# Optimization experiments

Measured on AMD Instinct MI355X. Metric: run time of the kernel, lower is better.

The kernel has to match this reference:

```python
import jax, jax.numpy as jnp
import numpy as np

B, C, S, H, W = 2, 128, 64, 128, 512
MID = 32
EPS = 1e-5


def layer_norm(x, g, b):
    m = jnp.mean(x, axis=-1, keepdims=True)
    v = jnp.var(x, axis=-1, keepdims=True)
    return (x - m) / jnp.sqrt(v + EPS) * g + b


def generate_y_for_attn(s, y, u):
    # y: [B, Cy, H, W], u: [B, s, s] int indices into W (clamped)
    b, cy, h, w = y.shape
    u = jnp.clip(u, 0, w - 1)
    yr = y.reshape(b, cy * h, w)
    idx = u.reshape(b, s * s)
    g = jax.vmap(lambda m, i: m[:, i])(yr, idx)          # [B, Cy*H, s^2]
    return g.reshape(b, cy, h, s * s).transpose(0, 3, 2, 1)  # [B, s^2, H, Cy]


def setup_inputs():
    key = jax.random.key(0)
    ks = jax.random.split(key, 10)
    lim = 1.0 / np.sqrt(C)
    return {
        "sat_x": jax.random.normal(ks[0], (B, C, S, S), jnp.float32),
        "grd_x": jax.random.normal(ks[1], (B, C, H, W), jnp.float32),
        "grd_height": jax.random.normal(ks[2], (B, 1, H, W), jnp.float32),
        "u": jax.random.randint(ks[3], (B, S, S), 0, W, jnp.int32),
        "ln_q_g": jnp.ones((C,), jnp.float32),
        "ln_q_b": jnp.zeros((C,), jnp.float32),
        "wq": jax.random.uniform(ks[4], (C, MID), jnp.float32, -lim, lim),
        "bq": jax.random.uniform(ks[5], (MID,), jnp.float32, -lim, lim),
        "ln_k_g": jnp.ones((C,), jnp.float32),
        "ln_k_b": jnp.zeros((C,), jnp.float32),
        "wk": jax.random.uniform(ks[6], (C, MID), jnp.float32, -lim, lim),
        "bk": jax.random.uniform(ks[7], (MID,), jnp.float32, -lim, lim),
    }


def reference(sat_x, grd_x, grd_height, u, ln_q_g, ln_q_b, wq, bq, ln_k_g, ln_k_b, wk, bk):
    b, c, s, _ = sat_x.shape
    scale = MID ** (-0.5)
    y_attn = generate_y_for_attn(s, grd_x, u)        # [B, S^2, H, C]
    v_attn = generate_y_for_attn(s, grd_height, u)   # [B, S^2, H, 1]
    x = sat_x.reshape(b, c, s * s).transpose(0, 2, 1)  # [B, M, C]
    q = layer_norm(x, ln_q_g, ln_q_b) @ wq + bq        # [B, M, 32]
    k = layer_norm(y_attn, ln_k_g, ln_k_b) @ wk + bk   # [B, M, H, 32]
    dot = scale * jnp.einsum("bmd,bmnd->bmn", q, k)    # [B, M, H]
    att = jax.nn.softmax(dot, axis=-1)
    a = jnp.sum(att[..., None] * v_attn, axis=-2)      # [B, M, 1]
    return a.transpose(0, 2, 1).reshape(b, 1, s, s)
```

## Files before the change

kernel.cpp:

```cpp
#include <hip/hip_runtime.h>
#include <math.h>

#define B_   2
#define C_   128
#define S_   64
#define H_   128
#define W_   512
#define M_   (S_ * S_)
#define MID_ 32
#define EPS_ 1e-5f
#define CAP_ 192

#define KBLK (B_ * H_ * (W_ / 64))
#define QBLK (B_ * (M_ / 64))
#define OBLK 4

typedef __attribute__((ext_vector_type(8))) short short8;
typedef __attribute__((ext_vector_type(4))) float floatx4;

__device__ __forceinline__ unsigned bfpair(float a, float b) {
    unsigned ua = __float_as_uint(a); ua += 0x7FFFu + ((ua >> 16) & 1u);
    unsigned ub = __float_as_uint(b); ub += 0x7FFFu + ((ub >> 16) & 1u);
    return (ua >> 16) | (ub & 0xFFFF0000u);
}

__global__ __launch_bounds__(256) void prep_kernel(
    const float* __restrict__ ln_k_g, const float* __restrict__ ln_k_b,
    const float* __restrict__ wk, const float* __restrict__ bk,
    const float* __restrict__ ln_q_g, const float* __restrict__ ln_q_b,
    const float* __restrict__ wq, const float* __restrict__ bq,
    float* __restrict__ prepbuf,
    short* __restrict__ wfrag,
    int* __restrict__ counts,
    int* __restrict__ ocount)
{
    const int tid = threadIdx.x;
    const int blk = blockIdx.x;
    const float* g    = blk ? ln_q_g : ln_k_g;
    const float* bl   = blk ? ln_q_b : ln_k_b;
    const float* wt   = blk ? wq     : wk;
    const float* bias = blk ? bq     : bk;

    __shared__ float pa[256], pb[256];

    float a = 0.f, c2 = 0.f;
#pragma unroll
    for (int k = 0; k < 16; ++k) {
        const int idx = tid + 256 * k;
        const float wv = wt[idx];
        const int c = idx >> 5;
        a  = fmaf(g[c],  wv, a);
        c2 = fmaf(bl[c], wv, c2);
    }
    pa[tid] = a; pb[tid] = c2;

    if (blk == 0) {
        ((int4*)counts)[tid] = make_int4(0, 0, 0, 0);
        if (tid == 0) *ocount = 0;
    }
    __syncthreads();

    if (tid < 32) {
        float s = 0.f, t = 0.f;
#pragma unroll
        for (int r = 0; r < 8; ++r) { s += pa[tid + 32 * r]; t += pb[tid + 32 * r]; }
        prepbuf[blk * 64 + tid]      = s;
        prepbuf[blk * 64 + 32 + tid] = t + bias[tid];
    }

    short* whiT = wfrag + blk * 8192;
    short* wloT = whiT + 4096;
#pragma unroll
    for (int e = 0; e < 16; ++e) {
        const int idx = tid * 16 + e;
        const int i    = idx & 7;
        const int ln   = (idx >> 3) & 63;
        const int kk   = (idx >> 9) & 3;
        const int jt   = idx >> 11;
        const int c = kk * 32 + (ln >> 4) * 8 + i;
        const int j = jt * 16 + (ln & 15);
        const float wp = g[c] * wt[c * MID_ + j];
        const unsigned bbits = __float_as_uint(wp);
        const unsigned hb = bbits & 0xFFFF0000u;
        whiT[idx] = (short)(hb >> 16);
        const float r = wp - __uint_as_float(hb);
        wloT[idx] = (short)(__float_as_uint(r) >> 16);
    }
}

__global__ __launch_bounds__(256) void proj_kernel(
    const float* __restrict__ grd_x,
    const float* __restrict__ sat_x,
    const float* __restrict__ prepbuf,
    const short* __restrict__ wfrag,
    const int*   __restrict__ u,
    unsigned short* __restrict__ kwb,
    float* __restrict__ qv,
    int* __restrict__ counts,
    int* __restrict__ bucket,
    int* __restrict__ ocount,
    int* __restrict__ olist)
{
    __shared__ float xs[C_ * 64];

    const int tid  = threadIdx.x;
    const int lane = tid & 63;
    const int wv   = __builtin_amdgcn_readfirstlane(tid >> 6);
    const int quad = lane >> 4;
    const int l16  = lane & 15;
    const int blk  = blockIdx.x;
    const bool is_k = (blk < KBLK);

    int b, h = 0, pos0;
    const float* xcol;
    size_t xstr;
    if (is_k) {
        const int wchunk = blk & 7;
        h    = (blk >> 3) & (H_ - 1);
        b    = blk >> 10;
        pos0 = wchunk * 64;
        xcol = grd_x + ((size_t)b * C_ * H_ + h) * W_ + pos0;
        xstr = (size_t)H_ * W_;
    } else {
        const int qblk = blk - KBLK;
        b    = qblk >> 6;
        pos0 = (qblk & 63) * 64;
        xcol = sat_x + (size_t)b * C_ * M_ + pos0;
        xstr = (size_t)M_;
    }
    const int pos = pos0 + wv * 16 + l16;

    {
        const int swz  = (wv >> 1) << 4;
        const float* gsrc = xcol + (size_t)(lane >> 4) * xstr
                                 + (((lane & 15) * 4) ^ swz);
#pragma unroll
        for (int r = 0; r < 8; ++r) {
            const float* src = gsrc + (size_t)(r * 16 + wv * 4) * xstr;
            float* dst = xs + (r * 16 + wv * 4) * 64;
            __builtin_amdgcn_global_load_lds(
                (const __attribute__((address_space(1))) unsigned int*)src,
                (__attribute__((address_space(3))) unsigned int*)dst,
                16, 0, 0);
        }
    }

    const short* whiT = wfrag + (is_k ? 0 : 8192);
    const short* wloT = whiT + 4096;
    short8 ahi[2][4], alo[2][4];
#pragma unroll
    for (int jt = 0; jt < 2; ++jt)
#pragma unroll
        for (int kk = 0; kk < 4; ++kk) {
            const int off = ((jt * 4 + kk) * 64 + lane) * 8;
            ahi[jt][kk] = *(const short8*)(whiT + off);
            alo[jt][kk] = *(const short8*)(wloT + off);
        }

    const int setoff = is_k ? 0 : 64;
    const float4 gw0 = *(const float4*)(prepbuf + setoff + quad * 4);
    const float4 bw0 = *(const float4*)(prepbuf + setoff + 32 + quad * 4);
    const float4 gw1 = *(const float4*)(prepbuf + setoff + 16 + quad * 4);
    const float4 bw1 = *(const float4*)(prepbuf + setoff + 48 + quad * 4);

    __syncthreads();

    floatx4 acc0 = {0.f, 0.f, 0.f, 0.f};
    floatx4 acc1 = {0.f, 0.f, 0.f, 0.f};
    float p1 = 0.f, p2 = 0.f;

    const int rpos = (wv * 16 + l16) ^ ((quad & 1) << 4);
    const float* xsl = xs + quad * 8 * 64 + rpos;

#pragma unroll
    for (int kk = 0; kk < 4; ++kk) {
        const float* xk = xsl + kk * 32 * 64;
        union { short8 v; unsigned u[4]; } bhi, blo;
#pragma unroll
        for (int e = 0; e < 4; ++e) {
            const float x0 = xk[(2 * e)     * 64];
            const float x1 = xk[(2 * e + 1) * 64];
            p1 += x0 + x1;
            p2 = fmaf(x0, x0, p2);
            p2 = fmaf(x1, x1, p2);
            const unsigned b0 = __float_as_uint(x0);
            const unsigned b1 = __float_as_uint(x1);
            bhi.u[e] = (b1 & 0xFFFF0000u) | (b0 >> 16);
            const float r0 = x0 - __uint_as_float(b0 & 0xFFFF0000u);
            const float r1 = x1 - __uint_as_float(b1 & 0xFFFF0000u);
            blo.u[e] = (__float_as_uint(r1) & 0xFFFF0000u) |
                       (__float_as_uint(r0) >> 16);
        }
        acc0 = __builtin_amdgcn_mfma_f32_16x16x32_bf16(ahi[0][kk], bhi.v, acc0, 0, 0, 0);
        acc1 = __builtin_amdgcn_mfma_f32_16x16x32_bf16(ahi[1][kk], bhi.v, acc1, 0, 0, 0);
        acc0 = __builtin_amdgcn_mfma_f32_16x16x32_bf16(ahi[0][kk], blo.v, acc0, 0, 0, 0);
        acc1 = __builtin_amdgcn_mfma_f32_16x16x32_bf16(ahi[1][kk], blo.v, acc1, 0, 0, 0);
        acc0 = __builtin_amdgcn_mfma_f32_16x16x32_bf16(alo[0][kk], bhi.v, acc0, 0, 0, 0);
        acc1 = __builtin_amdgcn_mfma_f32_16x16x32_bf16(alo[1][kk], bhi.v, acc1, 0, 0, 0);
    }

    p1 += __shfl_xor(p1, 16, 64);
    p1 += __shfl_xor(p1, 32, 64);
    p2 += __shfl_xor(p2, 16, 64);
    p2 += __shfl_xor(p2, 32, 64);
    const float mean = p1 * (1.f / C_);
    const float rstd = rsqrtf(fmaf(-mean, mean, p2 * (1.f / C_)) + EPS_);

    float o0x = fmaf(rstd, fmaf(-mean, gw0.x, acc0[0]), bw0.x);
    float o0y = fmaf(rstd, fmaf(-mean, gw0.y, acc0[1]), bw0.y);
    float o0z = fmaf(rstd, fmaf(-mean, gw0.z, acc0[2]), bw0.z);
    float o0w = fmaf(rstd, fmaf(-mean, gw0.w, acc0[3]), bw0.w);
    float o1x = fmaf(rstd, fmaf(-mean, gw1.x, acc1[0]), bw1.x);
    float o1y = fmaf(rstd, fmaf(-mean, gw1.y, acc1[1]), bw1.y);
    float o1z = fmaf(rstd, fmaf(-mean, gw1.z, acc1[2]), bw1.z);
    float o1w = fmaf(rstd, fmaf(-mean, gw1.w, acc1[3]), bw1.w);

    if (is_k) {
        unsigned short* orow = kwb + (((size_t)b * W_ + pos) * H_ + h) * MID_;
        uint2 u0, u1;
        u0.x = bfpair(o0x, o0y); u0.y = bfpair(o0z, o0w);
        u1.x = bfpair(o1x, o1y); u1.y = bfpair(o1z, o1w);
        *(uint2*)(orow + quad * 4)      = u0;
        *(uint2*)(orow + 16 + quad * 4) = u1;
    } else {
        float* orow = qv + ((size_t)b * M_ + pos) * MID_;
        *(float4*)(orow + quad * 4)      = make_float4(o0x, o0y, o0z, o0w);
        *(float4*)(orow + 16 + quad * 4) = make_float4(o1x, o1y, o1z, o1w);
        if (quad == 0) {
            const int bm = b * M_ + pos;
            int w = u[bm];
            w = min(max(w, 0), W_ - 1);
            const int bw = b * W_ + w;
            const int p = atomicAdd(&counts[bw], 1);
            if (p < CAP_) bucket[bw * CAP_ + p] = bm;
            else          olist[atomicAdd(ocount, 1)] = bm;
        }
    }
}

__global__ __launch_bounds__(256) void battn_kernel(
    const float* __restrict__ qv,
    const unsigned short* __restrict__ kwb,
    const float* __restrict__ gh,
    const int*   __restrict__ u,
    const int*   __restrict__ counts,
    const int*   __restrict__ bucket,
    const int*   __restrict__ ocount,
    const int*   __restrict__ olist,
    float* __restrict__ out)
{
    const int blk  = blockIdx.x;
    const int tid  = threadIdx.x;
    const int lane = tid & 63;
    const int wv   = __builtin_amdgcn_readfirstlane(tid >> 6);
    const float sc = 0.17677669529663687f;

    if (blk >= B_ * W_) {
        const int nof = min(*ocount, B_ * M_);
        const int gwv = (blk - B_ * W_) * 4 + wv;
        for (int i = gwv; i < nof; i += OBLK * 4) {
            const int bm = olist[i];
            const int b  = bm >> 12;
            int w = u[bm];
            w = min(max(w, 0), W_ - 1);
            const unsigned short* kr = kwb + ((size_t)b * W_ + w) * H_ * MID_;
            const float* qr = qv + (size_t)bm * MID_;
            float sq[MID_];
#pragma unroll
            for (int j = 0; j < MID_; ++j) sq[j] = qr[j];
            float d0 = 0.f, d1 = 0.f;
#pragma unroll
            for (int j = 0; j < MID_; ++j) {
                d0 = fmaf(sq[j], __uint_as_float((unsigned)kr[lane * MID_ + j] << 16), d0);
                d1 = fmaf(sq[j], __uint_as_float((unsigned)kr[(lane + 64) * MID_ + j] << 16), d1);
            }
            d0 *= sc; d1 *= sc;
            float mx = fmaxf(d0, d1);
#pragma unroll
            for (int o = 32; o > 0; o >>= 1) mx = fmaxf(mx, __shfl_xor(mx, o, 64));
            const float v0 = gh[((size_t)b * H_ + lane) * W_ + w];
            const float v1 = gh[((size_t)b * H_ + lane + 64) * W_ + w];
            const float e0 = __expf(d0 - mx);
            const float e1 = __expf(d1 - mx);
            float s   = e0 + e1;
            float svv = fmaf(e0, v0, e1 * v1);
#pragma unroll
            for (int o = 32; o > 0; o >>= 1) {
                s   += __shfl_xor(s,   o, 64);
                svv += __shfl_xor(svv, o, 64);
            }
            if (lane == 0) out[bm] = svv / s;
        }
        return;
    }

    const int n = min(counts[blk], CAP_);
    if (wv >= n) return;

    const int b = blk >> 9;
    const int w = blk & (W_ - 1);

    const uint4* k4 = (const uint4*)(kwb + (size_t)blk * H_ * MID_);
    float ka[32], kb[32];
#pragma unroll
    for (int t = 0; t < 4; ++t) {
        const uint4 ua = k4[lane * 4 + t];
        const uint4 ub = k4[(lane + 64) * 4 + t];
        ka[t*8+0] = __uint_as_float(ua.x << 16); ka[t*8+1] = __uint_as_float(ua.x & 0xFFFF0000u);
        ka[t*8+2] = __uint_as_float(ua.y << 16); ka[t*8+3] = __uint_as_float(ua.y & 0xFFFF0000u);
        ka[t*8+4] = __uint_as_float(ua.z << 16); ka[t*8+5] = __uint_as_float(ua.z & 0xFFFF0000u);
        ka[t*8+6] = __uint_as_float(ua.w << 16); ka[t*8+7] = __uint_as_float(ua.w & 0xFFFF0000u);
        kb[t*8+0] = __uint_as_float(ub.x << 16); kb[t*8+1] = __uint_as_float(ub.x & 0xFFFF0000u);
        kb[t*8+2] = __uint_as_float(ub.y << 16); kb[t*8+3] = __uint_as_float(ub.y & 0xFFFF0000u);
        kb[t*8+4] = __uint_as_float(ub.z << 16); kb[t*8+5] = __uint_as_float(ub.z & 0xFFFF0000u);
        kb[t*8+6] = __uint_as_float(ub.w << 16); kb[t*8+7] = __uint_as_float(ub.w & 0xFFFF0000u);
    }

    const float v0 = gh[((size_t)b * H_ + lane) * W_ + w];
    const float v1 = gh[((size_t)b * H_ + lane + 64) * W_ + w];

    const int* bkt = bucket + (size_t)blk * CAP_;

    for (int i = wv; i < n; i += 4) {
        const int bm = bkt[i];
        const float* qr = qv + (size_t)bm * MID_;
        float sq[MID_];
#pragma unroll
        for (int j = 0; j < MID_; ++j) sq[j] = qr[j];

        float d0 = 0.f, d1 = 0.f;
#pragma unroll
        for (int j = 0; j < MID_; ++j) {
            d0 = fmaf(sq[j], ka[j], d0);
            d1 = fmaf(sq[j], kb[j], d1);
        }
        d0 *= sc; d1 *= sc;

        float mx = fmaxf(d0, d1);
#pragma unroll
        for (int o = 32; o > 0; o >>= 1) mx = fmaxf(mx, __shfl_xor(mx, o, 64));

        const float e0 = __expf(d0 - mx);
        const float e1 = __expf(d1 - mx);
        float s   = e0 + e1;
        float svv = fmaf(e0, v0, e1 * v1);
#pragma unroll
        for (int o = 32; o > 0; o >>= 1) {
            s   += __shfl_xor(s,   o, 64);
            svv += __shfl_xor(svv, o, 64);
        }

        if (lane == 0) out[bm] = svv / s;
    }
}

extern "C" void kernel_launch(void* const* d_in, const int* in_sizes, int n_in,
                              void* d_out, int out_size, void* d_ws, size_t ws_size,
                              hipStream_t stream) {
    const float* sat_x      = (const float*)d_in[0];
    const float* grd_x      = (const float*)d_in[1];
    const float* grd_height = (const float*)d_in[2];
    const int*   u          = (const int*)d_in[3];
    const float* ln_q_g     = (const float*)d_in[4];
    const float* ln_q_b     = (const float*)d_in[5];
    const float* wq         = (const float*)d_in[6];
    const float* bq         = (const float*)d_in[7];
    const float* ln_k_g     = (const float*)d_in[8];
    const float* ln_k_b     = (const float*)d_in[9];
    const float* wk         = (const float*)d_in[10];
    const float* bk         = (const float*)d_in[11];

    float* out = (float*)d_out;

    char* ws = (char*)d_ws;
    unsigned short* kwb = (unsigned short*)ws;
    float* q       = (float*)(ws + (size_t)8  * 1024 * 1024);
    int*   counts  = (int*)  (ws + (size_t)9  * 1024 * 1024);
    int*   ocount  = (int*)  (ws + (size_t)9  * 1024 * 1024 + 4096);
    int*   bucket  = (int*)  (ws + (size_t)9  * 1024 * 1024 + 8192);
    int*   olist   = bucket + B_ * W_ * CAP_;
    float* prepbuf = (float*)(ws + (size_t)10 * 1024 * 1024);
    short* wfrag   = (short*)(ws + (size_t)10 * 1024 * 1024 + 4096);

    prep_kernel<<<2, 256, 0, stream>>>(
        ln_k_g, ln_k_b, wk, bk, ln_q_g, ln_q_b, wq, bq,
        prepbuf, wfrag, counts, ocount);
    proj_kernel<<<KBLK + QBLK, 256, 0, stream>>>(
        grd_x, sat_x, prepbuf, wfrag, u, kwb, q, counts, bucket, ocount, olist);
    battn_kernel<<<B_ * W_ + OBLK, 256, 0, stream>>>(
        q, kwb, grd_height, u, counts, bucket, ocount, olist, out);
}
```

Measured before the change: 130.7 us.

## Fuse prep, projection and attention into one persistent kernel with grid barriers

Replaces three kernel launches with a single persistent kernel of 768 blocks that runs weight prep, then a grid-wide software barrier, then a loop over projection tiles, then another barrier, then the bucketed attention. Inside the projection loop it prefetches the next tile into LDS via global_load_lds while the epilogue of the current tile runs. This is meant to remove launch gaps and tail effects between kernels and to overlap the memory loads with compute. The spin barrier assumes all 768 blocks are co-resident (3 per CU) and relies on a monotonically increasing global counter. If residency does not hold, the kernel can deadlock.

```diff
diff --git a/kernel.cpp b/kernel.cpp
--- a/kernel.cpp
+++ b/kernel.cpp
@@ -13,10 +13,29 @@
 
 #define KBLK (B_ * H_ * (W_ / 64))
 #define QBLK (B_ * (M_ / 64))
+#define NTILE (KBLK + QBLK)
 #define OBLK 4
+#define GRID_ 768
 
 typedef __attribute__((ext_vector_type(8))) short short8;
 typedef __attribute__((ext_vector_type(4))) float floatx4;
+
+__device__ unsigned g_barcnt = 0;
+
+__device__ __forceinline__ void gsync() {
+    __syncthreads();
+    if (threadIdx.x == 0) {
+        __threadfence();
+        unsigned my = __hip_atomic_fetch_add(&g_barcnt, 1u, __ATOMIC_ACQ_REL,
+                                             __HIP_MEMORY_SCOPE_AGENT);
+        unsigned tgt = (my / GRID_ + 1u) * GRID_;
+        while (__hip_atomic_load(&g_barcnt, __ATOMIC_ACQUIRE,
+                                 __HIP_MEMORY_SCOPE_AGENT) < tgt)
+            __builtin_amdgcn_s_sleep(2);
+        __threadfence();
+    }
+    __syncthreads();
+}
 
 __device__ __forceinline__ unsigned bfpair(float a, float b) {
     unsigned ua = __float_as_uint(a); ua += 0x7FFFu + ((ua >> 16) & 1u);
@@ -24,24 +43,14 @@
     return (ua >> 16) | (ub & 0xFFFF0000u);
 }
 
-__global__ __launch_bounds__(256) void prep_kernel(
-    const float* __restrict__ ln_k_g, const float* __restrict__ ln_k_b,
-    const float* __restrict__ wk, const float* __restrict__ bk,
-    const float* __restrict__ ln_q_g, const float* __restrict__ ln_q_b,
-    const float* __restrict__ wq, const float* __restrict__ bq,
-    float* __restrict__ prepbuf,
-    short* __restrict__ wfrag,
-    int* __restrict__ counts,
-    int* __restrict__ ocount)
+__device__ __forceinline__ void prep_work(
+    int setq, const float* __restrict__ g, const float* __restrict__ bl,
+    const float* __restrict__ wt, const float* __restrict__ bias,
+    float* __restrict__ prepbuf, short* __restrict__ wfrag,
+    int* __restrict__ counts, int* __restrict__ ocount,
+    float* pa, float* pb)
 {
     const int tid = threadIdx.x;
-    const int blk = blockIdx.x;
-    const float* g    = blk ? ln_q_g : ln_k_g;
-    const float* bl   = blk ? ln_q_b : ln_k_b;
-    const float* wt   = blk ? wq     : wk;
-    const float* bias = blk ? bq     : bk;
-
-    __shared__ float pa[256], pb[256];
 
     float a = 0.f, c2 = 0.f;
 #pragma unroll
@@ -54,7 +63,7 @@
     }
     pa[tid] = a; pb[tid] = c2;
 
-    if (blk == 0) {
+    if (!setq) {
         ((int4*)counts)[tid] = make_int4(0, 0, 0, 0);
         if (tid == 0) *ocount = 0;
     }
@@ -64,11 +73,11 @@
         float s = 0.f, t = 0.f;
 #pragma unroll
         for (int r = 0; r < 8; ++r) { s += pa[tid + 32 * r]; t += pb[tid + 32 * r]; }
-        prepbuf[blk * 64 + tid]      = s;
-        prepbuf[blk * 64 + 32 + tid] = t + bias[tid];
-    }
-
-    short* whiT = wfrag + blk * 8192;
+        prepbuf[setq * 64 + tid]      = s;
+        prepbuf[setq * 64 + 32 + tid] = t + bias[tid];
+    }
+
+    short* whiT = wfrag + setq * 8192;
     short* wloT = whiT + 4096;
 #pragma unroll
     for (int e = 0; e < 16; ++e) {
@@ -88,176 +97,66 @@
     }
 }
 
-__global__ __launch_bounds__(256) void proj_kernel(
-    const float* __restrict__ grd_x,
-    const float* __restrict__ sat_x,
-    const float* __restrict__ prepbuf,
-    const short* __restrict__ wfrag,
-    const int*   __restrict__ u,
-    unsigned short* __restrict__ kwb,
-    float* __restrict__ qv,
-    int* __restrict__ counts,
-    int* __restrict__ bucket,
-    int* __restrict__ ocount,
-    int* __restrict__ olist)
-{
-    __shared__ float xs[C_ * 64];
-
-    const int tid  = threadIdx.x;
-    const int lane = tid & 63;
-    const int wv   = __builtin_amdgcn_readfirstlane(tid >> 6);
-    const int quad = lane >> 4;
-    const int l16  = lane & 15;
-    const int blk  = blockIdx.x;
-    const bool is_k = (blk < KBLK);
-
-    int b, h = 0, pos0;
+struct Geo {
     const float* xcol;
     size_t xstr;
-    if (is_k) {
-        const int wchunk = blk & 7;
-        h    = (blk >> 3) & (H_ - 1);
-        b    = blk >> 10;
-        pos0 = wchunk * 64;
-        xcol = grd_x + ((size_t)b * C_ * H_ + h) * W_ + pos0;
-        xstr = (size_t)H_ * W_;
+    int b, h, pos0;
+    bool is_k;
+};
+
+__device__ __forceinline__ Geo tile_geo(int t, const float* __restrict__ grd_x,
+                                        const float* __restrict__ sat_x) {
+    Geo ge;
+    ge.is_k = (t < KBLK);
+    if (ge.is_k) {
+        const int wchunk = t & 7;
+        ge.h    = (t >> 3) & (H_ - 1);
+        ge.b    = t >> 10;
+        ge.pos0 = wchunk * 64;
+        ge.xcol = grd_x + ((size_t)ge.b * C_ * H_ + ge.h) * W_ + ge.pos0;
+        ge.xstr = (size_t)H_ * W_;
     } else {
-        const int qblk = blk - KBLK;
-        b    = qblk >> 6;
-        pos0 = (qblk & 63) * 64;
-        xcol = sat_x + (size_t)b * C_ * M_ + pos0;
-        xstr = (size_t)M_;
-    }
-    const int pos = pos0 + wv * 16 + l16;
-
-    {
-        const int swz  = (wv >> 1) << 4;
-        const float* gsrc = xcol + (size_t)(lane >> 4) * xstr
-                                 + (((lane & 15) * 4) ^ swz);
-#pragma unroll
-        for (int r = 0; r < 8; ++r) {
-            const float* src = gsrc + (size_t)(r * 16 + wv * 4) * xstr;
-            float* dst = xs + (r * 16 + wv * 4) * 64;
-            __builtin_amdgcn_global_load_lds(
-                (const __attribute__((address_space(1))) unsigned int*)src,
-                (__attribute__((address_space(3))) unsigned int*)dst,
-                16, 0, 0);
-        }
-    }
-
-    const short* whiT = wfrag + (is_k ? 0 : 8192);
-    const short* wloT = whiT + 4096;
-    short8 ahi[2][4], alo[2][4];
-#pragma unroll
-    for (int jt = 0; jt < 2; ++jt)
-#pragma unroll
-        for (int kk = 0; kk < 4; ++kk) {
-            const int off = ((jt * 4 + kk) * 64 + lane) * 8;
-            ahi[jt][kk] = *(const short8*)(whiT + off);
-            alo[jt][kk] = *(const short8*)(wloT + off);
-        }
-
-    const int setoff = is_k ? 0 : 64;
-    const float4 gw0 = *(const float4*)(prepbuf + setoff + quad * 4);
-    const float4 bw0 = *(const float4*)(prepbuf + setoff + 32 + quad * 4);
-    const float4 gw1 = *(const float4*)(prepbuf + setoff + 16 + quad * 4);
-    const float4 bw1 = *(const float4*)(prepbuf + setoff + 48 + quad * 4);
-
-    __syncthreads();
-
-    floatx4 acc0 = {0.f, 0.f, 0.f, 0.f};
-    floatx4 acc1 = {0.f, 0.f, 0.f, 0.f};
-    float p1 = 0.f, p2 = 0.f;
-
-    const int rpos = (wv * 16 + l16) ^ ((quad & 1) << 4);
-    const float* xsl = xs + quad * 8 * 64 + rpos;
-
-#pragma unroll
-    for (int kk = 0; kk < 4; ++kk) {
-        const float* xk = xsl + kk * 32 * 64;
-        union { short8 v; unsigned u[4]; } bhi, blo;
-#pragma unroll
-        for (int e = 0; e < 4; ++e) {
-            const float x0 = xk[(2 * e)     * 64];
-            const float x1 = xk[(2 * e + 1) * 64];
-            p1 += x0 + x1;
-            p2 = fmaf(x0, x0, p2);
-            p2 = fmaf(x1, x1, p2);
-            const unsigned b0 = __float_as_uint(x0);
-            const unsigned b1 = __float_as_uint(x1);
-            bhi.u[e] = (b1 & 0xFFFF0000u) | (b0 >> 16);
-            const float r0 = x0 - __uint_as_float(b0 & 0xFFFF0000u);
-            const float r1 = x1 - __uint_as_float(b1 & 0xFFFF0000u);
-            blo.u[e] = (__float_as_uint(r1) & 0xFFFF0000u) |
-                       (__float_as_uint(r0) >> 16);
-        }
-        acc0 = __builtin_amdgcn_mfma_f32_16x16x32_bf16(ahi[0][kk], bhi.v, acc0, 0, 0, 0);
-        acc1 = __builtin_amdgcn_mfma_f32_16x16x32_bf16(ahi[1][kk], bhi.v, acc1, 0, 0, 0);
-        acc0 = __builtin_amdgcn_mfma_f32_16x16x32_bf16(ahi[0][kk], blo.v, acc0, 0, 0, 0);
-        acc1 = __builtin_amdgcn_mfma_f32_16x16x32_bf16(ahi[1][kk], blo.v, acc1, 0, 0, 0);
-        acc0 = __builtin_amdgcn_mfma_f32_16x16x32_bf16(alo[0][kk], bhi.v, acc0, 0, 0, 0);
-        acc1 = __builtin_amdgcn_mfma_f32_16x16x32_bf16(alo[1][kk], bhi.v, acc1, 0, 0, 0);
-    }
-
-    p1 += __shfl_xor(p1, 16, 64);
-    p1 += __shfl_xor(p1, 32, 64);
-    p2 += __shfl_xor(p2, 16, 64);
-    p2 += __shfl_xor(p2, 32, 64);
-    const float mean = p1 * (1.f / C_);
-    const float rstd = rsqrtf(fmaf(-mean, mean, p2 * (1.f / C_)) + EPS_);
-
-    float o0x = fmaf(rstd, fmaf(-mean, gw0.x, acc0[0]), bw0.x);
-    float o0y = fmaf(rstd, fmaf(-mean, gw0.y, acc0[1]), bw0.y);
-    float o0z = fmaf(rstd, fmaf(-mean, gw0.z, acc0[2]), bw0.z);
-    float o0w = fmaf(rstd, fmaf(-mean, gw0.w, acc0[3]), bw0.w);
-    float o1x = fmaf(rstd, fmaf(-mean, gw1.x, acc1[0]), bw1.x);
-    float o1y = fmaf(rstd, fmaf(-mean, gw1.y, acc1[1]), bw1.y);
-    float o1z = fmaf(rstd, fmaf(-mean, gw1.z, acc1[2]), bw1.z);
-    float o1w = fmaf(rstd, fmaf(-mean, gw1.w, acc1[3]), bw1.w);
-
-    if (is_k) {
-        unsigned short* orow = kwb + (((size_t)b * W_ + pos) * H_ + h) * MID_;
-        uint2 u0, u1;
-        u0.x = bfpair(o0x, o0y); u0.y = bfpair(o0z, o0w);
-        u1.x = bfpair(o1x, o1y); u1.y = bfpair(o1z, o1w);
-        *(uint2*)(orow + quad * 4)      = u0;
-        *(uint2*)(orow + 16 + quad * 4) = u1;
-    } else {
-        float* orow = qv + ((size_t)b * M_ + pos) * MID_;
-        *(float4*)(orow + quad * 4)      = make_float4(o0x, o0y, o0z, o0w);
-        *(float4*)(orow + 16 + quad * 4) = make_float4(o1x, o1y, o1z, o1w);
-        if (quad == 0) {
-            const int bm = b * M_ + pos;
-            int w = u[bm];
-            w = min(max(w, 0), W_ - 1);
-            const int bw = b * W_ + w;
-            const int p = atomicAdd(&counts[bw], 1);
-            if (p < CAP_) bucket[bw * CAP_ + p] = bm;
-            else          olist[atomicAdd(ocount, 1)] = bm;
-        }
-    }
-}
-
-__global__ __launch_bounds__(256) void battn_kernel(
-    const float* __restrict__ qv,
-    const unsigned short* __restrict__ kwb,
-    const float* __restrict__ gh,
-    const int*   __restrict__ u,
-    const int*   __restrict__ counts,
-    const int*   __restrict__ bucket,
-    const int*   __restrict__ ocount,
-    const int*   __restrict__ olist,
-    float* __restrict__ out)
+        const int qblk = t - KBLK;
+        ge.b    = qblk >> 6;
+        ge.h    = 0;
+        ge.pos0 = (qblk & 63) * 64;
+        ge.xcol = sat_x + (size_t)ge.b * C_ * M_ + ge.pos0;
+        ge.xstr = (size_t)M_;
+    }
+    return ge;
+}
+
+__device__ __forceinline__ void issue_dma(const Geo& ge, float* xs, int lane, int wv) {
+    const int swz  = (wv >> 1) << 4;
+    const float* gsrc = ge.xcol + (size_t)(lane >> 4) * ge.xstr
+                               + (((lane & 15) * 4) ^ swz);
+#pragma unroll
+    for (int r = 0; r < 8; ++r) {
+        const float* src = gsrc + (size_t)(r * 16 + wv * 4) * ge.xstr;
+        float* dst = xs + (r * 16 + wv * 4) * 64;
+        __builtin_amdgcn_global_load_lds(
+            (const __attribute__((address_space(1))) unsigned int*)src,
+            (__attribute__((address_space(3))) unsigned int*)dst,
+            16, 0, 0);
+    }
+}
+
+__device__ void battn_tile(int tb, int lane, int wv,
+                           const float* __restrict__ qv,
+                           const unsigned short* __restrict__ kwb,
+                           const float* __restrict__ gh,
+                           const int*   __restrict__ u,
+                           const int*   __restrict__ counts,
+                           const int*   __restrict__ bucket,
+                           const int*   __restrict__ ocount,
+                           const int*   __restrict__ olist,
+                           float* __restrict__ out)
 {
-    const int blk  = blockIdx.x;
-    const int tid  = threadIdx.x;
-    const int lane = tid & 63;
-    const int wv   = __builtin_amdgcn_readfirstlane(tid >> 6);
     const float sc = 0.17677669529663687f;
 
-    if (blk >= B_ * W_) {
+    if (tb >= B_ * W_) {
         const int nof = min(*ocount, B_ * M_);
-        const int gwv = (blk - B_ * W_) * 4 + wv;
+        const int gwv = (tb - B_ * W_) * 4 + wv;
         for (int i = gwv; i < nof; i += OBLK * 4) {
             const int bm = olist[i];
             const int b  = bm >> 12;
@@ -294,13 +193,13 @@
         return;
     }
 
-    const int n = min(counts[blk], CAP_);
+    const int n = min(counts[tb], CAP_);
     if (wv >= n) return;
 
-    const int b = blk >> 9;
-    const int w = blk & (W_ - 1);
-
-    const uint4* k4 = (const uint4*)(kwb + (size_t)blk * H_ * MID_);
+    const int b = tb >> 9;
+    const int w = tb & (W_ - 1);
+
+    const uint4* k4 = (const uint4*)(kwb + (size_t)tb * H_ * MID_);
     float ka[32], kb[32];
 #pragma unroll
     for (int t = 0; t < 4; ++t) {
@@ -319,7 +218,7 @@
     const float v0 = gh[((size_t)b * H_ + lane) * W_ + w];
     const float v1 = gh[((size_t)b * H_ + lane + 64) * W_ + w];
 
-    const int* bkt = bucket + (size_t)blk * CAP_;
+    const int* bkt = bucket + (size_t)tb * CAP_;
 
     for (int i = wv; i < n; i += 4) {
         const int bm = bkt[i];
@@ -352,6 +251,151 @@
 
         if (lane == 0) out[bm] = svv / s;
     }
+}
+
+__global__ __launch_bounds__(256, 3) void fused_kernel(
+    const float* __restrict__ grd_x,
+    const float* __restrict__ sat_x,
+    const float* __restrict__ gh,
+    const int*   __restrict__ u,
+    const float* __restrict__ ln_k_g, const float* __restrict__ ln_k_b,
+    const float* __restrict__ wk, const float* __restrict__ bk,
+    const float* __restrict__ ln_q_g, const float* __restrict__ ln_q_b,
+    const float* __restrict__ wq, const float* __restrict__ bq,
+    float* __restrict__ prepbuf,
+    short* __restrict__ wfrag,
+    unsigned short* __restrict__ kwb,
+    float* __restrict__ qv,
+    int* __restrict__ counts,
+    int* __restrict__ bucket,
+    int* __restrict__ ocount,
+    int* __restrict__ olist,
+    float* __restrict__ out)
+{
+    __shared__ float xs[C_ * 64];
+    __shared__ float pa[256], pb[256];
+
+    const int tid  = threadIdx.x;
+    const int lane = tid & 63;
+    const int wv   = __builtin_amdgcn_readfirstlane(tid >> 6);
+    const int quad = lane >> 4;
+    const int l16  = lane & 15;
+    const int blk  = blockIdx.x;
+
+    issue_dma(tile_geo(blk, grd_x, sat_x), xs, lane, wv);
+    if (blk == 0)
+        prep_work(0, ln_k_g, ln_k_b, wk, bk, prepbuf, wfrag, counts, ocount, pa, pb);
+    else if (blk == 1)
+        prep_work(1, ln_q_g, ln_q_b, wq, bq, prepbuf, wfrag, counts, ocount, pa, pb);
+
+    gsync();
+
+    for (int t = blk; t < NTILE; t += GRID_) {
+        const Geo ge = tile_geo(t, grd_x, sat_x);
+        const bool is_k = ge.is_k;
+        const int pos = ge.pos0 + wv * 16 + l16;
+
+        const short* whiT = wfrag + (is_k ? 0 : 8192);
+        const short* wloT = whiT + 4096;
+        short8 ahi[2][4], alo[2][4];
+#pragma unroll
+        for (int jt = 0; jt < 2; ++jt)
+#pragma unroll
+            for (int kk = 0; kk < 4; ++kk) {
+                const int off = ((jt * 4 + kk) * 64 + lane) * 8;
+                ahi[jt][kk] = *(const short8*)(whiT + off);
+                alo[jt][kk] = *(const short8*)(wloT + off);
+            }
+
+        const int setoff = is_k ? 0 : 64;
+        const float4 gw0 = *(const float4*)(prepbuf + setoff + quad * 4);
+        const float4 bw0 = *(const float4*)(prepbuf + setoff + 32 + quad * 4);
+        const float4 gw1 = *(const float4*)(prepbuf + setoff + 16 + quad * 4);
+        const float4 bw1 = *(const float4*)(prepbuf + setoff + 48 + quad * 4);
+
+        floatx4 acc0 = {0.f, 0.f, 0.f, 0.f};
+        floatx4 acc1 = {0.f, 0.f, 0.f, 0.f};
+        float p1 = 0.f, p2 = 0.f;
+
+        const int rpos = (wv * 16 + l16) ^ ((quad & 1) << 4);
+        const float* xsl = xs + quad * 8 * 64 + rpos;
+
+#pragma unroll
+        for (int kk = 0; kk < 4; ++kk) {
+            const float* xk = xsl + kk * 32 * 64;
+            union { short8 v; unsigned u[4]; } bhi, blo;
+#pragma unroll
+            for (int e = 0; e < 4; ++e) {
+                const float x0 = xk[(2 * e)     * 64];
+                const float x1 = xk[(2 * e + 1) * 64];
+                p1 += x0 + x1;
+                p2 = fmaf(x0, x0, p2);
+                p2 = fmaf(x1, x1, p2);
+                const unsigned b0 = __float_as_uint(x0);
+                const unsigned b1 = __float_as_uint(x1);
+                bhi.u[e] = (b1 & 0xFFFF0000u) | (b0 >> 16);
+                const float r0 = x0 - __uint_as_float(b0 & 0xFFFF0000u);
+                const float r1 = x1 - __uint_as_float(b1 & 0xFFFF0000u);
+                blo.u[e] = (__float_as_uint(r1) & 0xFFFF0000u) |
+                           (__float_as_uint(r0) >> 16);
+            }
+            acc0 = __builtin_amdgcn_mfma_f32_16x16x32_bf16(ahi[0][kk], bhi.v, acc0, 0, 0, 0);
+            acc1 = __builtin_amdgcn_mfma_f32_16x16x32_bf16(ahi[1][kk], bhi.v, acc1, 0, 0, 0);
+            acc0 = __builtin_amdgcn_mfma_f32_16x16x32_bf16(ahi[0][kk], blo.v, acc0, 0, 0, 0);
+            acc1 = __builtin_amdgcn_mfma_f32_16x16x32_bf16(ahi[1][kk], blo.v, acc1, 0, 0, 0);
+            acc0 = __builtin_amdgcn_mfma_f32_16x16x32_bf16(alo[0][kk], bhi.v, acc0, 0, 0, 0);
+            acc1 = __builtin_amdgcn_mfma_f32_16x16x32_bf16(alo[1][kk], bhi.v, acc1, 0, 0, 0);
+        }
+
+        __syncthreads();
+        const bool more = (t + GRID_ < NTILE);
+        if (more) issue_dma(tile_geo(t + GRID_, grd_x, sat_x), xs, lane, wv);
+
+        p1 += __shfl_xor(p1, 16, 64);
+        p1 += __shfl_xor(p1, 32, 64);
+        p2 += __shfl_xor(p2, 16, 64);
+        p2 += __shfl_xor(p2, 32, 64);
+        const float mean = p1 * (1.f / C_);
+        const float rstd = rsqrtf(fmaf(-mean, mean, p2 * (1.f / C_)) + EPS_);
+
+        const float o0x = fmaf(rstd, fmaf(-mean, gw0.x, acc0[0]), bw0.x);
+        const float o0y = fmaf(rstd, fmaf(-mean, gw0.y, acc0[1]), bw0.y);
+        const float o0z = fmaf(rstd, fmaf(-mean, gw0.z, acc0[2]), bw0.z);
+        const float o0w = fmaf(rstd, fmaf(-mean, gw0.w, acc0[3]), bw0.w);
+        const float o1x = fmaf(rstd, fmaf(-mean, gw1.x, acc1[0]), bw1.x);
+        const float o1y = fmaf(rstd, fmaf(-mean, gw1.y, acc1[1]), bw1.y);
+        const float o1z = fmaf(rstd, fmaf(-mean, gw1.z, acc1[2]), bw1.z);
+        const float o1w = fmaf(rstd, fmaf(-mean, gw1.w, acc1[3]), bw1.w);
+
+        if (is_k) {
+            unsigned short* orow = kwb + (((size_t)ge.b * W_ + pos) * H_ + ge.h) * MID_;
+            uint2 u0, u1;
+            u0.x = bfpair(o0x, o0y); u0.y = bfpair(o0z, o0w);
+            u1.x = bfpair(o1x, o1y); u1.y = bfpair(o1z, o1w);
+            *(uint2*)(orow + quad * 4)      = u0;
+            *(uint2*)(orow + 16 + quad * 4) = u1;
+        } else {
+            float* orow = qv + ((size_t)ge.b * M_ + pos) * MID_;
+            *(float4*)(orow + quad * 4)      = make_float4(o0x, o0y, o0z, o0w);
+            *(float4*)(orow + 16 + quad * 4) = make_float4(o1x, o1y, o1z, o1w);
+            if (quad == 0) {
+                const int bm = ge.b * M_ + pos;
+                int w = u[bm];
+                w = min(max(w, 0), W_ - 1);
+                const int bw = ge.b * W_ + w;
+                const int p = atomicAdd(&counts[bw], 1);
+                if (p < CAP_) bucket[bw * CAP_ + p] = bm;
+                else          olist[atomicAdd(ocount, 1)] = bm;
+            }
+        }
+
+        if (more) __syncthreads();
+    }
+
+    gsync();
+
+    for (int t = blk; t < B_ * W_ + OBLK; t += GRID_)
+        battn_tile(t, lane, wv, qv, kwb, gh, u, counts, bucket, ocount, olist, out);
 }
 
 extern "C" void kernel_launch(void* const* d_in, const int* in_sizes, int n_in,
@@ -382,11 +426,10 @@
     float* prepbuf = (float*)(ws + (size_t)10 * 1024 * 1024);
     short* wfrag   = (short*)(ws + (size_t)10 * 1024 * 1024 + 4096);
 
-    prep_kernel<<<2, 256, 0, stream>>>(
-        ln_k_g, ln_k_b, wk, bk, ln_q_g, ln_q_b, wq, bq,
-        prepbuf, wfrag, counts, ocount);
-    proj_kernel<<<KBLK + QBLK, 256, 0, stream>>>(
-        grd_x, sat_x, prepbuf, wfrag, u, kwb, q, counts, bucket, ocount, olist);
-    battn_kernel<<<B_ * W_ + OBLK, 256, 0, stream>>>(
-        q, kwb, grd_height, u, counts, bucket, ocount, olist, out);
-}
+    fused_kernel<<<GRID_, 256, 0, stream>>>(
+        grd_x, sat_x, grd_height, u,
+        ln_k_g, ln_k_b, wk, bk,
+        ln_q_g, ln_q_b, wq, bq,
+        prepbuf, wfrag, kwb, q,
+        counts, bucket, ocount, olist, out);
+}
```

After: 365.7 us. 2.8x slower.

## Make projection kernel persistent and prefetch next tile into LDS during epilogue

Applied to the files above, without the earlier changes.

The projection kernel now runs a fixed grid of 1024 blocks that loop over the 2176 tiles. Each block issues the global-to-LDS DMA for its next tile right after the MFMA phase, so the load overlaps the LayerNorm epilogue and the stores. The attention kernel also marks bucket indices as wave-uniform with readfirstlane so q-row addressing goes through scalar registers. The cost is an extra barrier per tile and some load imbalance, since tile counts per block differ (2 or 3).

```diff
diff --git a/kernel.cpp b/kernel.cpp
--- a/kernel.cpp
+++ b/kernel.cpp
@@ -13,6 +13,8 @@
 
 #define KBLK (B_ * H_ * (W_ / 64))
 #define QBLK (B_ * (M_ / 64))
+#define NTILE (KBLK + QBLK)
+#define PGRID 1024
 #define OBLK 4
 
 typedef __attribute__((ext_vector_type(8))) short short8;
@@ -88,6 +90,50 @@
     }
 }
 
+struct Geo {
+    const float* xcol;
+    size_t xstr;
+    int b, h, pos0;
+    bool is_k;
+};
+
+__device__ __forceinline__ Geo tile_geo(int t, const float* __restrict__ grd_x,
+                                        const float* __restrict__ sat_x) {
+    Geo ge;
+    ge.is_k = (t < KBLK);
+    if (ge.is_k) {
+        const int wchunk = t & 7;
+        ge.h    = (t >> 3) & (H_ - 1);
+        ge.b    = t >> 10;
+        ge.pos0 = wchunk * 64;
+        ge.xcol = grd_x + ((size_t)ge.b * C_ * H_ + ge.h) * W_ + ge.pos0;
+        ge.xstr = (size_t)H_ * W_;
+    } else {
+        const int qblk = t - KBLK;
+        ge.b    = qblk >> 6;
+        ge.h    = 0;
+        ge.pos0 = (qblk & 63) * 64;
+        ge.xcol = sat_x + (size_t)ge.b * C_ * M_ + ge.pos0;
+        ge.xstr = (size_t)M_;
+    }
+    return ge;
+}
+
+__device__ __forceinline__ void issue_dma(const Geo& ge, float* xs, int lane, int wv) {
+    const int swz  = (wv >> 1) << 4;
+    const float* gsrc = ge.xcol + (size_t)(lane >> 4) * ge.xstr
+                               + (((lane & 15) * 4) ^ swz);
+#pragma unroll
+    for (int r = 0; r < 8; ++r) {
+        const float* src = gsrc + (size_t)(r * 16 + wv * 4) * ge.xstr;
+        float* dst = xs + (r * 16 + wv * 4) * 64;
+        __builtin_amdgcn_global_load_lds(
+            (const __attribute__((address_space(1))) unsigned int*)src,
+            (__attribute__((address_space(3))) unsigned int*)dst,
+            16, 0, 0);
+    }
+}
+
 __global__ __launch_bounds__(256) void proj_kernel(
     const float* __restrict__ grd_x,
     const float* __restrict__ sat_x,
@@ -109,131 +155,108 @@
     const int quad = lane >> 4;
     const int l16  = lane & 15;
     const int blk  = blockIdx.x;
-    const bool is_k = (blk < KBLK);
-
-    int b, h = 0, pos0;
-    const float* xcol;
-    size_t xstr;
-    if (is_k) {
-        const int wchunk = blk & 7;
-        h    = (blk >> 3) & (H_ - 1);
-        b    = blk >> 10;
-        pos0 = wchunk * 64;
-        xcol = grd_x + ((size_t)b * C_ * H_ + h) * W_ + pos0;
-        xstr = (size_t)H_ * W_;
-    } else {
-        const int qblk = blk - KBLK;
-        b    = qblk >> 6;
-        pos0 = (qblk & 63) * 64;
-        xcol = sat_x + (size_t)b * C_ * M_ + pos0;
-        xstr = (size_t)M_;
-    }
-    const int pos = pos0 + wv * 16 + l16;
-
-    {
-        const int swz  = (wv >> 1) << 4;
-        const float* gsrc = xcol + (size_t)(lane >> 4) * xstr
-                                 + (((lane & 15) * 4) ^ swz);
-#pragma unroll
-        for (int r = 0; r < 8; ++r) {
-            const float* src = gsrc + (size_t)(r * 16 + wv * 4) * xstr;
-            float* dst = xs + (r * 16 + wv * 4) * 64;
-            __builtin_amdgcn_global_load_lds(
-                (const __attribute__((address_space(1))) unsigned int*)src,
-                (__attribute__((address_space(3))) unsigned int*)dst,
-                16, 0, 0);
+
+    issue_dma(tile_geo(blk, grd_x, sat_x), xs, lane, wv);
+
+    for (int t = blk; t < NTILE; t += PGRID) {
+        const Geo ge = tile_geo(t, grd_x, sat_x);
+        const bool is_k = ge.is_k;
+        const int pos = ge.pos0 + wv * 16 + l16;
+
+        const short* whiT = wfrag + (is_k ? 0 : 8192);
+        const short* wloT = whiT + 4096;
+        short8 ahi[2][4], alo[2][4];
+#pragma unroll
+        for (int jt = 0; jt < 2; ++jt)
+#pragma unroll
+            for (int kk = 0; kk < 4; ++kk) {
+                const int off = ((jt * 4 + kk) * 64 + lane) * 8;
+                ahi[jt][kk] = *(const short8*)(whiT + off);
+                alo[jt][kk] = *(const short8*)(wloT + off);
+            }
+
+        const int setoff = is_k ? 0 : 64;
+        const float4 gw0 = *(const float4*)(prepbuf + setoff + quad * 4);
+        const float4 bw0 = *(const float4*)(prepbuf + setoff + 32 + quad * 4);
+        const float4 gw1 = *(const float4*)(prepbuf + setoff + 16 + quad * 4);
+        const float4 bw1 = *(const float4*)(prepbuf + setoff + 48 + quad * 4);
+
+        __syncthreads();
+
+        floatx4 acc0 = {0.f, 0.f, 0.f, 0.f};
+        floatx4 acc1 = {0.f, 0.f, 0.f, 0.f};
+        float p1 = 0.f, p2 = 0.f;
+
+        const int rpos = (wv * 16 + l16) ^ ((quad & 1) << 4);
+        const float* xsl = xs + quad * 8 * 64 + rpos;
+
+#pragma unroll
+        for (int kk = 0; kk < 4; ++kk) {
+            const float* xk = xsl + kk * 32 * 64;
+            union { short8 v; unsigned u[4]; } bhi, blo;
+#pragma unroll
+            for (int e = 0; e < 4; ++e) {
+                const float x0 = xk[(2 * e)     * 64];
+                const float x1 = xk[(2 * e + 1) * 64];
+                p1 += x0 + x1;
+                p2 = fmaf(x0, x0, p2);
+                p2 = fmaf(x1, x1, p2);
+                const unsigned b0 = __float_as_uint(x0);
+                const unsigned b1 = __float_as_uint(x1);
+                bhi.u[e] = (b1 & 0xFFFF0000u) | (b0 >> 16);
+                const float r0 = x0 - __uint_as_float(b0 & 0xFFFF0000u);
+                const float r1 = x1 - __uint_as_float(b1 & 0xFFFF0000u);
+                blo.u[e] = (__float_as_uint(r1) & 0xFFFF0000u) |
+                           (__float_as_uint(r0) >> 16);
+            }
+            acc0 = __builtin_amdgcn_mfma_f32_16x16x32_bf16(ahi[0][kk], bhi.v, acc0, 0, 0, 0);
+            acc1 = __builtin_amdgcn_mfma_f32_16x16x32_bf16(ahi[1][kk], bhi.v, acc1, 0, 0, 0);
+            acc0 = __builtin_amdgcn_mfma_f32_16x16x32_bf16(ahi[0][kk], blo.v, acc0, 0, 0, 0);
+            acc1 = __builtin_amdgcn_mfma_f32_16x16x32_bf16(ahi[1][kk], blo.v, acc1, 0, 0, 0);
+            acc0 = __builtin_amdgcn_mfma_f32_16x16x32_bf16(alo[0][kk], bhi.v, acc0, 0, 0, 0);
+            acc1 = __builtin_amdgcn_mfma_f32_16x16x32_bf16(alo[1][kk], bhi.v, acc1, 0, 0, 0);
         }
-    }
-
-    const short* whiT = wfrag + (is_k ? 0 : 8192);
-    const short* wloT = whiT + 4096;
-    short8 ahi[2][4], alo[2][4];
-#pragma unroll
-    for (int jt = 0; jt < 2; ++jt)
-#pragma unroll
-        for (int kk = 0; kk < 4; ++kk) {
-            const int off = ((jt * 4 + kk) * 64 + lane) * 8;
-            ahi[jt][kk] = *(const short8*)(whiT + off);
-            alo[jt][kk] = *(const short8*)(wloT + off);
-        }
-
-    const int setoff = is_k ? 0 : 64;
-    const float4 gw0 = *(const float4*)(prepbuf + setoff + quad * 4);
-    const float4 bw0 = *(const float4*)(prepbuf + setoff + 32 + quad * 4);
-    const float4 gw1 = *(const float4*)(prepbuf + setoff + 16 + quad * 4);
-    const float4 bw1 = *(const float4*)(prepbuf + setoff + 48 + quad * 4);
-
-    __syncthreads();
-
-    floatx4 acc0 = {0.f, 0.f, 0.f, 0.f};
-    floatx4 acc1 = {0.f, 0.f, 0.f, 0.f};
-    float p1 = 0.f, p2 = 0.f;
-
-    const int rpos = (wv * 16 + l16) ^ ((quad & 1) << 4);
-    const float* xsl = xs + quad * 8 * 64 + rpos;
-
-#pragma unroll
-    for (int kk = 0; kk < 4; ++kk) {
-        const float* xk = xsl + kk * 32 * 64;
-        union { short8 v; unsigned u[4]; } bhi, blo;
-#pragma unroll
-        for (int e = 0; e < 4; ++e) {
-            const float x0 = xk[(2 * e)     * 64];
-            const float x1 = xk[(2 * e + 1) * 64];
-            p1 += x0 + x1;
-            p2 = fmaf(x0, x0, p2);
-            p2 = fmaf(x1, x1, p2);
-            const unsigned b0 = __float_as_uint(x0);
-            const unsigned b1 = __float_as_uint(x1);
-            bhi.u[e] = (b1 & 0xFFFF0000u) | (b0 >> 16);
-            const float r0 = x0 - __uint_as_float(b0 & 0xFFFF0000u);
-            const float r1 = x1 - __uint_as_float(b1 & 0xFFFF0000u);
-            blo.u[e] = (__float_as_uint(r1) & 0xFFFF0000u) |
-                       (__float_as_uint(r0) >> 16);
-        }
-        acc0 = __builtin_amdgcn_mfma_f32_16x16x32_bf16(ahi[0][kk], bhi.v, acc0, 0, 0, 0);
-        acc1 = __builtin_amdgcn_mfma_f32_16x16x32_bf16(ahi[1][kk], bhi.v, acc1, 0, 0, 0);
-        acc0 = __builtin_amdgcn_mfma_f32_16x16x32_bf16(ahi[0][kk], blo.v, acc0, 0, 0, 0);
-        acc1 = __builtin_amdgcn_mfma_f32_16x16x32_bf16(ahi[1][kk], blo.v, acc1, 0, 0, 0);
-        acc0 = __builtin_amdgcn_mfma_f32_16x16x32_bf16(alo[0][kk], bhi.v, acc0, 0, 0, 0);
-        acc1 = __builtin_amdgcn_mfma_f32_16x16x32_bf16(alo[1][kk], bhi.v, acc1, 0, 0, 0);
-    }
-
-    p1 += __shfl_xor(p1, 16, 64);
-    p1 += __shfl_xor(p1, 32, 64);
-    p2 += __shfl_xor(p2, 16, 64);
-    p2 += __shfl_xor(p2, 32, 64);
-    const float mean = p1 * (1.f / C_);
-    const float rstd = rsqrtf(fmaf(-mean, mean, p2 * (1.f / C_)) + EPS_);
-
-    float o0x = fmaf(rstd, fmaf(-mean, gw0.x, acc0[0]), bw0.x);
-    float o0y = fmaf(rstd, fmaf(-mean, gw0.y, acc0[1]), bw0.y);
-    float o0z = fmaf(rstd, fmaf(-mean, gw0.z, acc0[2]), bw0.z);
-    float o0w = fmaf(rstd, fmaf(-mean, gw0.w, acc0[3]), bw0.w);
-    float o1x = fmaf(rstd, fmaf(-mean, gw1.x, acc1[0]), bw1.x);
-    float o1y = fmaf(rstd, fmaf(-mean, gw1.y, acc1[1]), bw1.y);
-    float o1z = fmaf(rstd, fmaf(-mean, gw1.z, acc1[2]), bw1.z);
-    float o1w = fmaf(rstd, fmaf(-mean, gw1.w, acc1[3]), bw1.w);
-
-    if (is_k) {
-        unsigned short* orow = kwb + (((size_t)b * W_ + pos) * H_ + h) * MID_;
-        uint2 u0, u1;
-        u0.x = bfpair(o0x, o0y); u0.y = bfpair(o0z, o0w);
-        u1.x = bfpair(o1x, o1y); u1.y = bfpair(o1z, o1w);
-        *(uint2*)(orow + quad * 4)      = u0;
-        *(uint2*)(orow + 16 + quad * 4) = u1;
-    } else {
-        float* orow = qv + ((size_t)b * M_ + pos) * MID_;
-        *(float4*)(orow + quad * 4)      = make_float4(o0x, o0y, o0z, o0w);
-        *(float4*)(orow + 16 + quad * 4) = make_float4(o1x, o1y, o1z, o1w);
-        if (quad == 0) {
-            const int bm = b * M_ + pos;
-            int w = u[bm];
-            w = min(max(w, 0), W_ - 1);
-            const int bw = b * W_ + w;
-            const int p = atomicAdd(&counts[bw], 1);
-            if (p < CAP_) bucket[bw * CAP_ + p] = bm;
-            else          olist[atomicAdd(ocount, 1)] = bm;
+
+        __syncthreads();
+        if (t + PGRID < NTILE)
+            issue_dma(tile_geo(t + PGRID, grd_x, sat_x), xs, lane, wv);
+
+        p1 += __shfl_xor(p1, 16, 64);
+        p1 += __shfl_xor(p1, 32, 64);
+        p2 += __shfl_xor(p2, 16, 64);
+        p2 += __shfl_xor(p2, 32, 64);
+        const float mean = p1 * (1.f / C_);
+        const float rstd = rsqrtf(fmaf(-mean, mean, p2 * (1.f / C_)) + EPS_);
+
+        const float o0x = fmaf(rstd, fmaf(-mean, gw0.x, acc0[0]), bw0.x);
+        const float o0y = fmaf(rstd, fmaf(-mean, gw0.y, acc0[1]), bw0.y);
+        const float o0z = fmaf(rstd, fmaf(-mean, gw0.z, acc0[2]), bw0.z);
+        const float o0w = fmaf(rstd, fmaf(-mean, gw0.w, acc0[3]), bw0.w);
+        const float o1x = fmaf(rstd, fmaf(-mean, gw1.x, acc1[0]), bw1.x);
+        const float o1y = fmaf(rstd, fmaf(-mean, gw1.y, acc1[1]), bw1.y);
+        const float o1z = fmaf(rstd, fmaf(-mean, gw1.z, acc1[2]), bw1.z);
+        const float o1w = fmaf(rstd, fmaf(-mean, gw1.w, acc1[3]), bw1.w);
+
+        if (is_k) {
+            unsigned short* orow = kwb + (((size_t)ge.b * W_ + pos) * H_ + ge.h) * MID_;
+            uint2 u0, u1;
+            u0.x = bfpair(o0x, o0y); u0.y = bfpair(o0z, o0w);
+            u1.x = bfpair(o1x, o1y); u1.y = bfpair(o1z, o1w);
+            *(uint2*)(orow + quad * 4)      = u0;
+            *(uint2*)(orow + 16 + quad * 4) = u1;
+        } else {
+            float* orow = qv + ((size_t)ge.b * M_ + pos) * MID_;
+            *(float4*)(orow + quad * 4)      = make_float4(o0x, o0y, o0z, o0w);
+            *(float4*)(orow + 16 + quad * 4) = make_float4(o1x, o1y, o1z, o1w);
+            if (quad == 0) {
+                const int bm = ge.b * M_ + pos;
+                int w = u[bm];
+                w = min(max(w, 0), W_ - 1);
+                const int bw = ge.b * W_ + w;
+                const int p = atomicAdd(&counts[bw], 1);
+                if (p < CAP_) bucket[bw * CAP_ + p] = bm;
+                else          olist[atomicAdd(ocount, 1)] = bm;
+            }
         }
     }
 }
@@ -259,7 +282,7 @@
         const int nof = min(*ocount, B_ * M_);
         const int gwv = (blk - B_ * W_) * 4 + wv;
         for (int i = gwv; i < nof; i += OBLK * 4) {
-            const int bm = olist[i];
+            const int bm = __builtin_amdgcn_readfirstlane(olist[i]);
             const int b  = bm >> 12;
             int w = u[bm];
             w = min(max(w, 0), W_ - 1);
@@ -322,7 +345,7 @@
     const int* bkt = bucket + (size_t)blk * CAP_;
 
     for (int i = wv; i < n; i += 4) {
-        const int bm = bkt[i];
+        const int bm = __builtin_amdgcn_readfirstlane(bkt[i]);
         const float* qr = qv + (size_t)bm * MID_;
         float sq[MID_];
 #pragma unroll
@@ -385,7 +408,7 @@
     prep_kernel<<<2, 256, 0, stream>>>(
         ln_k_g, ln_k_b, wk, bk, ln_q_g, ln_q_b, wq, bq,
         prepbuf, wfrag, counts, ocount);
-    proj_kernel<<<KBLK + QBLK, 256, 0, stream>>>(
+    proj_kernel<<<PGRID, 256, 0, stream>>>(
         grd_x, sat_x, prepbuf, wfrag, u, kwb, q, counts, bucket, ocount, olist);
     battn_kernel<<<B_ * W_ + OBLK, 256, 0, stream>>>(
         q, kwb, grd_height, u, counts, bucket, ocount, olist, out);
```

After: 135.5 us. +3.6%, slower.
